# Kernel tuning notes

Measured on AMD Instinct MI355X. Metric: run time of the kernel, lower is better.

The kernel has to match this reference:

```python
import jax, jax.numpy as jnp
import numpy as np

R_SELF = 0.1  # config.r_self from the 'GENERAL' preset


def setup_inputs() -> dict:
    key = jax.random.key(0)
    k1, k2 = jax.random.split(key)
    N, M, D = 16384, 8192, 128
    x = jax.random.uniform(k1, (N, D), dtype=jnp.float32)
    self_samples = jax.random.uniform(k2, (M, D), dtype=jnp.float32)
    return {"x": x, "self_samples": self_samples}


def _cdist(a, b):
    # Euclidean pairwise distances, same math as torch.cdist(p=2).
    a2 = jnp.sum(a * a, axis=1, keepdims=True)          # [N,1]
    b2 = jnp.sum(b * b, axis=1)[None, :]                # [1,M]
    d2 = a2 + b2 - 2.0 * (a @ b.T)                      # [N,M]
    return jnp.sqrt(jnp.maximum(d2, 0.0))


def reference(x, self_samples):
    # get_anomaly_score: min over self set, shifted by r_self, clamped at 0.
    min_dist_to_self = jnp.min(_cdist(x, self_samples), axis=1)  # [N]
    score = jnp.maximum(min_dist_to_self - R_SELF, 0.0)
    return score
```

## Files before the change

kernel.cpp:

```cpp
#include <hip/hip_runtime.h>


using half_t = _Float16;
typedef _Float16 half8 __attribute__((ext_vector_type(8)));
typedef _Float16 half2v __attribute__((ext_vector_type(2)));
typedef float floatx16 __attribute__((ext_vector_type(16)));

#define TILE_ELEMS (128 * 128)

__device__ __forceinline__ void async_load16(const void* g, void* l) {
    __builtin_amdgcn_global_load_lds(
        (const __attribute__((address_space(1))) void*)g,
        (__attribute__((address_space(3))) void*)l, 16, 0, 0);
}

__device__ __forceinline__ void stage_tile(const half_t* __restrict__ Bt,
                                           half_t* __restrict__ dst, int tid) {
    #pragma unroll
    for (int j = 0; j < 4; ++j) {
        int chunk = j * 512 + tid;
        async_load16(Bt + (size_t)chunk * 8, dst + (size_t)chunk * 8);
    }
}

__device__ __forceinline__ half2v h2min(half2v a, half2v b) {
    return __builtin_elementwise_min(a, b);
}

__device__ __forceinline__ half2v pkrtz(float lo, float hi) {
    auto t = __builtin_amdgcn_cvt_pkrtz(lo, hi);
    return __builtin_bit_cast(half2v, t);
}

__global__ __launch_bounds__(256) void prep_kernel(
    const float* __restrict__ x, const float* __restrict__ self,
    half_t* __restrict__ Aws, half_t* __restrict__ Bws,
    float* __restrict__ b2h, float* __restrict__ a2, int Atiles)
{
    __shared__ float part[256];
    int tile = blockIdx.x;
    int tid  = threadIdx.x;
    bool isB = tile >= Atiles;
    int bt   = tile - Atiles;
    const float* src = isB ? (self + (size_t)bt * TILE_ELEMS)
                           : (x    + (size_t)tile * TILE_ELEMS);
    half_t* dst = isB ? (Bws + (size_t)bt * TILE_ELEMS)
                      : (Aws + (size_t)tile * TILE_ELEMS);
    float sgn = isB ? 1.f : -1.f;

    int rowt = tid & 127;
    int k8b  = tid >> 7;
    float ss = 0.f;
    #pragma unroll
    for (int i = 0; i < 8; ++i) {
        int k8 = i * 2 + k8b;
        const float4* p = (const float4*)(src + rowt * 128 + k8 * 8);
        float4 f0 = p[0];
        float4 f1 = p[1];
        half8 h;
        h[0] = (half_t)(sgn * f0.x); h[1] = (half_t)(sgn * f0.y);
        h[2] = (half_t)(sgn * f0.z); h[3] = (half_t)(sgn * f0.w);
        h[4] = (half_t)(sgn * f1.x); h[5] = (half_t)(sgn * f1.y);
        h[6] = (half_t)(sgn * f1.z); h[7] = (half_t)(sgn * f1.w);
        *(half8*)(dst + (size_t)(i * 256 + tid) * 8) = h;
        ss += f0.x*f0.x + f0.y*f0.y + f0.z*f0.z + f0.w*f0.w;
        ss += f1.x*f1.x + f1.y*f1.y + f1.z*f1.z + f1.w*f1.w;
    }
    part[tid] = ss;
    __syncthreads();
    if (tid < 128) {
        float tot = part[tid] + part[tid + 128];
        if (isB) b2h[bt * 128 + tid] = 0.5f * tot;
        else     a2[tile * 128 + tid] = tot;
    }
}

template<int VN>
__device__ __forceinline__ void gemm_iter(
    int t, int iters, int tid, int wc, int ln31, int lh,
    const half_t* __restrict__ Bbase, half_t (*ring)[TILE_ELEMS],
    const float* __restrict__ b2sh,
    const half8 (&areg)[4][8], half2v (&minacc)[4][8])
{
    __builtin_amdgcn_sched_barrier(0);
    if constexpr (VN == 4) asm volatile("s_waitcnt vmcnt(4)" ::: "memory");
    else                   asm volatile("s_waitcnt vmcnt(0)" ::: "memory");
    asm volatile("s_waitcnt lgkmcnt(0)" ::: "memory");
    __builtin_amdgcn_s_barrier();
    __builtin_amdgcn_sched_barrier(0);

    if (t + 2 < iters)
        stage_tile(Bbase + (size_t)(t + 2) * TILE_ELEMS, &ring[(t + 2) % 3][0], tid);

    const half_t* Bs = &ring[t % 3][0];
    float b2v = b2sh[t * 128 + wc * 32 + ln31];

    half8 bf[8];
    #pragma unroll
    for (int ki = 0; ki < 8; ++ki)
        bf[ki] = *(const half8*)(Bs + (size_t)((ki * 2 + lh) * 128 + wc * 32 + ln31) * 8);

    floatx16 c0;
    #pragma unroll
    for (int r = 0; r < 16; ++r) c0[r] = b2v;

    #pragma unroll
    for (int rp = 0; rp < 2; ++rp) {
        floatx16 a0 = __builtin_amdgcn_mfma_f32_32x32x16_f16(areg[rp * 2][0],     bf[0], c0, 0, 0, 0);
        floatx16 a1 = __builtin_amdgcn_mfma_f32_32x32x16_f16(areg[rp * 2 + 1][0], bf[0], c0, 0, 0, 0);
        #pragma unroll
        for (int ki = 1; ki < 8; ++ki) {
            a0 = __builtin_amdgcn_mfma_f32_32x32x16_f16(areg[rp * 2][ki],     bf[ki], a0, 0, 0, 0);
            a1 = __builtin_amdgcn_mfma_f32_32x32x16_f16(areg[rp * 2 + 1][ki], bf[ki], a1, 0, 0, 0);
        }
        #pragma unroll
        for (int i = 0; i < 8; ++i) {
            minacc[rp * 2][i]     = h2min(minacc[rp * 2][i],     pkrtz(a0[2 * i], a0[2 * i + 1]));
            minacc[rp * 2 + 1][i] = h2min(minacc[rp * 2 + 1][i], pkrtz(a1[2 * i], a1[2 * i + 1]));
        }
    }
}

__global__ __launch_bounds__(512, 2) void min_gemm_kernel(
    const half_t* __restrict__ Aws, const half_t* __restrict__ Bws,
    const float* __restrict__ b2h, float* __restrict__ Pmin, int Mslice)
{
    __shared__ half_t ring[3][TILE_ELEMS];
    __shared__ float  b2sh[2048];

    int tid  = threadIdx.x;
    int lane = tid & 63;
    int wid  = tid >> 6;
    int wr   = wid >> 2;
    int wc   = wid & 3;
    int ln31 = lane & 31, lh = lane >> 5;

    const half_t* Atile = Aws + (size_t)(blockIdx.x * 2 + wr) * TILE_ELEMS;
    half8 areg[4][8];
    #pragma unroll
    for (int rt = 0; rt < 4; ++rt)
        #pragma unroll
        for (int ki = 0; ki < 8; ++ki)
            areg[rt][ki] = *(const half8*)(
                Atile + (size_t)((ki * 2 + lh) * 128 + rt * 32 + ln31) * 8);

    int s = blockIdx.y;
    for (int j = tid; j < Mslice; j += 512)
        b2sh[j] = b2h[s * Mslice + j];

    half2v minacc[4][8];
    const half_t HMAX = (half_t)65504.f;
    #pragma unroll
    for (int rt = 0; rt < 4; ++rt)
        #pragma unroll
        for (int i = 0; i < 8; ++i) { minacc[rt][i][0] = HMAX; minacc[rt][i][1] = HMAX; }

    int iters = Mslice >> 7;
    const half_t* Bbase = Bws + (size_t)s * iters * TILE_ELEMS;

    __syncthreads();

    stage_tile(Bbase,              &ring[0][0], tid);
    stage_tile(Bbase + TILE_ELEMS, &ring[1][0], tid);

    for (int t = 0; t < iters - 1; ++t)
        gemm_iter<4>(t, iters, tid, wc, ln31, lh, Bbase, ring, b2sh, areg, minacc);
    gemm_iter<0>(iters - 1, iters, tid, wc, ln31, lh, Bbase, ring, b2sh, areg, minacc);

    #pragma unroll
    for (int rt = 0; rt < 4; ++rt)
        #pragma unroll
        for (int i = 0; i < 8; ++i) {
            int m = __builtin_bit_cast(int, minacc[rt][i]);
            #pragma unroll
            for (int x = 1; x < 32; x <<= 1) {
                int o = __shfl_xor(m, x, 64);
                m = __builtin_bit_cast(int,
                        h2min(__builtin_bit_cast(half2v, m),
                              __builtin_bit_cast(half2v, o)));
            }
            if (ln31 == 0) {
                half2v mv = __builtin_bit_cast(half2v, m);
                int r0 = 2 * i, r1 = 2 * i + 1;
                int rowb = blockIdx.x * 256 + wr * 128 + rt * 32 + 4 * lh;
                int row0 = rowb + (r0 & 3) + 8 * (r0 >> 2);
                int row1 = rowb + (r1 & 3) + 8 * (r1 >> 2);
                Pmin[(size_t)row0 * 16 + s * 4 + wc] = (float)mv[0];
                Pmin[(size_t)row1 * 16 + s * 4 + wc] = (float)mv[1];
            }
        }
}

__global__ __launch_bounds__(256) void final_kernel(
    const float* __restrict__ a2, const float* __restrict__ Pmin,
    float* __restrict__ out)
{
    int row = blockIdx.x * 256 + threadIdx.x;
    const float4* pp = (const float4*)(Pmin + (size_t)row * 16);
    float4 p0 = pp[0];
    float4 p1 = pp[1];
    float4 p2 = pp[2];
    float4 p3 = pp[3];
    float q0 = fminf(fminf(p0.x, p0.y), fminf(p0.z, p0.w));
    float q1 = fminf(fminf(p1.x, p1.y), fminf(p1.z, p1.w));
    float q2 = fminf(fminf(p2.x, p2.y), fminf(p2.z, p2.w));
    float q3 = fminf(fminf(p3.x, p3.y), fminf(p3.z, p3.w));
    float p  = fminf(fminf(q0, q1), fminf(q2, q3));
    float d2 = a2[row] + 2.f * p;
    float d  = sqrtf(fmaxf(d2, 0.f));
    out[row] = fmaxf(d - 0.1f, 0.f);
}

extern "C" void kernel_launch(void* const* d_in, const int* in_sizes, int n_in,
                              void* d_out, int out_size, void* d_ws, size_t ws_size,
                              hipStream_t stream)
{
    const float* x    = (const float*)d_in[0];
    const float* self = (const float*)d_in[1];
    float* out        = (float*)d_out;

    int N = in_sizes[0] / 128;
    int M = in_sizes[1] / 128;
    int Atiles = N / 128;
    int Btiles = M / 128;

    char* w      = (char*)d_ws;
    half_t* Aws  = (half_t*)w;
    half_t* Bws  = Aws + (size_t)N * 128;
    float*  b2h  = (float*)(w + (size_t)(N + M) * 128 * 2);
    float*  Pmin = b2h + M;
    float*  a2   = Pmin + (size_t)N * 16;

    prep_kernel<<<Atiles + Btiles, 256, 0, stream>>>(x, self, Aws, Bws, b2h, a2, Atiles);

    int Mslice = M / 4;
    dim3 grid(N / 256, 4);
    min_gemm_kernel<<<grid, 512, 0, stream>>>(Aws, Bws, b2h, Pmin, Mslice);

    final_kernel<<<N / 256, 256, 0, stream>>>(a2, Pmin, out);
}
```

Before: 103.0 us.

## Double-buffer B fragments in registers, remap block IDs, and raise MFMA priority

```diff
diff --git a/kernel.cpp b/kernel.cpp
--- a/kernel.cpp
+++ b/kernel.cpp
@@ -7,6 +7,7 @@
 typedef float floatx16 __attribute__((ext_vector_type(16)));
 
 #define TILE_ELEMS (128 * 128)
+#define MFMA16 __builtin_amdgcn_mfma_f32_32x32x16_f16
 
 __device__ __forceinline__ void async_load16(const void* g, void* l) {
     __builtin_amdgcn_global_load_lds(
@@ -14,12 +15,12 @@
         (__attribute__((address_space(3))) void*)l, 16, 0, 0);
 }
 
-__device__ __forceinline__ void stage_tile(const half_t* __restrict__ Bt,
-                                           half_t* __restrict__ dst, int tid) {
-    #pragma unroll
-    for (int j = 0; j < 4; ++j) {
-        int chunk = j * 512 + tid;
-        async_load16(Bt + (size_t)chunk * 8, dst + (size_t)chunk * 8);
+__device__ __forceinline__ void stage4(const half_t* __restrict__ Bt,
+                                       half_t* __restrict__ dst, int tid) {
+    #pragma unroll
+    for (int p = 0; p < 4; ++p) {
+        int c = p * 512 + tid;
+        async_load16(Bt + (size_t)c * 8, dst + (size_t)c * 8);
     }
 }
 
@@ -75,50 +76,65 @@
     }
 }
 
-template<int VN>
-__device__ __forceinline__ void gemm_iter(
+__device__ __forceinline__ void body(
     int t, int iters, int tid, int wc, int ln31, int lh,
     const half_t* __restrict__ Bbase, half_t (*ring)[TILE_ELEMS],
     const float* __restrict__ b2sh,
+    half8 (&cur)[8], half8 (&nxt)[8], float& b2v,
     const half8 (&areg)[4][8], half2v (&minacc)[4][8])
 {
-    __builtin_amdgcn_sched_barrier(0);
-    if constexpr (VN == 4) asm volatile("s_waitcnt vmcnt(4)" ::: "memory");
-    else                   asm volatile("s_waitcnt vmcnt(0)" ::: "memory");
+    asm volatile("s_waitcnt vmcnt(0)" ::: "memory");
+    __builtin_amdgcn_sched_barrier(0);
+    __builtin_amdgcn_s_barrier();
+    __builtin_amdgcn_sched_barrier(0);
+
+    if (t + 2 < iters)
+        stage4(Bbase + (size_t)(t + 2) * TILE_ELEMS, &ring[(t + 2) % 3][0], tid);
+
+    float b2vn = b2v;
+    if (t + 1 < iters) {
+        const half_t* Bs = &ring[(t + 1) % 3][0];
+        #pragma unroll
+        for (int ki = 0; ki < 8; ++ki)
+            nxt[ki] = *(const half8*)(Bs + (size_t)((ki * 2 + lh) * 128 + wc * 32 + ln31) * 8);
+        b2vn = b2sh[(t + 1) * 128 + wc * 32 + ln31];
+    }
+
+    const floatx16 ZV = (floatx16)0.0f;
+
+    __builtin_amdgcn_s_setprio(1);
+    floatx16 acc0 = MFMA16(areg[0][0], cur[0], ZV, 0, 0, 0);
+    floatx16 acc1 = MFMA16(areg[1][0], cur[0], ZV, 0, 0, 0);
+    #pragma unroll
+    for (int ki = 1; ki < 8; ++ki) {
+        acc0 = MFMA16(areg[0][ki], cur[ki], acc0, 0, 0, 0);
+        acc1 = MFMA16(areg[1][ki], cur[ki], acc1, 0, 0, 0);
+    }
+    __builtin_amdgcn_s_setprio(0);
+    #pragma unroll
+    for (int i = 0; i < 8; ++i) {
+        minacc[0][i] = h2min(minacc[0][i], pkrtz(acc0[2*i] + b2v, acc0[2*i+1] + b2v));
+        minacc[1][i] = h2min(minacc[1][i], pkrtz(acc1[2*i] + b2v, acc1[2*i+1] + b2v));
+    }
+
+    __builtin_amdgcn_s_setprio(1);
+    floatx16 acc2 = MFMA16(areg[2][0], cur[0], ZV, 0, 0, 0);
+    floatx16 acc3 = MFMA16(areg[3][0], cur[0], ZV, 0, 0, 0);
+    #pragma unroll
+    for (int ki = 1; ki < 8; ++ki) {
+        acc2 = MFMA16(areg[2][ki], cur[ki], acc2, 0, 0, 0);
+        acc3 = MFMA16(areg[3][ki], cur[ki], acc3, 0, 0, 0);
+    }
+    __builtin_amdgcn_s_setprio(0);
+    #pragma unroll
+    for (int i = 0; i < 8; ++i) {
+        minacc[2][i] = h2min(minacc[2][i], pkrtz(acc2[2*i] + b2v, acc2[2*i+1] + b2v));
+        minacc[3][i] = h2min(minacc[3][i], pkrtz(acc3[2*i] + b2v, acc3[2*i+1] + b2v));
+    }
+
     asm volatile("s_waitcnt lgkmcnt(0)" ::: "memory");
-    __builtin_amdgcn_s_barrier();
-    __builtin_amdgcn_sched_barrier(0);
-
-    if (t + 2 < iters)
-        stage_tile(Bbase + (size_t)(t + 2) * TILE_ELEMS, &ring[(t + 2) % 3][0], tid);
-
-    const half_t* Bs = &ring[t % 3][0];
-    float b2v = b2sh[t * 128 + wc * 32 + ln31];
-
-    half8 bf[8];
-    #pragma unroll
-    for (int ki = 0; ki < 8; ++ki)
-        bf[ki] = *(const half8*)(Bs + (size_t)((ki * 2 + lh) * 128 + wc * 32 + ln31) * 8);
-
-    floatx16 c0;
-    #pragma unroll
-    for (int r = 0; r < 16; ++r) c0[r] = b2v;
-
-    #pragma unroll
-    for (int rp = 0; rp < 2; ++rp) {
-        floatx16 a0 = __builtin_amdgcn_mfma_f32_32x32x16_f16(areg[rp * 2][0],     bf[0], c0, 0, 0, 0);
-        floatx16 a1 = __builtin_amdgcn_mfma_f32_32x32x16_f16(areg[rp * 2 + 1][0], bf[0], c0, 0, 0, 0);
-        #pragma unroll
-        for (int ki = 1; ki < 8; ++ki) {
-            a0 = __builtin_amdgcn_mfma_f32_32x32x16_f16(areg[rp * 2][ki],     bf[ki], a0, 0, 0, 0);
-            a1 = __builtin_amdgcn_mfma_f32_32x32x16_f16(areg[rp * 2 + 1][ki], bf[ki], a1, 0, 0, 0);
-        }
-        #pragma unroll
-        for (int i = 0; i < 8; ++i) {
-            minacc[rp * 2][i]     = h2min(minacc[rp * 2][i],     pkrtz(a0[2 * i], a0[2 * i + 1]));
-            minacc[rp * 2 + 1][i] = h2min(minacc[rp * 2 + 1][i], pkrtz(a1[2 * i], a1[2 * i + 1]));
-        }
-    }
+    __builtin_amdgcn_sched_barrier(0);
+    b2v = b2vn;
 }
 
 __global__ __launch_bounds__(512, 2) void min_gemm_kernel(
@@ -135,7 +151,12 @@
     int wc   = wid & 3;
     int ln31 = lane & 31, lh = lane >> 5;
 
-    const half_t* Atile = Aws + (size_t)(blockIdx.x * 2 + wr) * TILE_ELEMS;
+    int id  = blockIdx.x + gridDim.x * blockIdx.y;
+    int swz = (id & 7) * 32 + (id >> 3);
+    int bx  = swz & 63;
+    int s   = swz >> 6;
+
+    const half_t* Atile = Aws + (size_t)(bx * 2 + wr) * TILE_ELEMS;
     half8 areg[4][8];
     #pragma unroll
     for (int rt = 0; rt < 4; ++rt)
@@ -144,8 +165,7 @@
             areg[rt][ki] = *(const half8*)(
                 Atile + (size_t)((ki * 2 + lh) * 128 + rt * 32 + ln31) * 8);
 
-    int s = blockIdx.y;
-    for (int j = tid; j < Mslice; j += 512)
+    for (int j = tid; j < 2048; j += 512)
         b2sh[j] = b2h[s * Mslice + j];
 
     half2v minacc[4][8];
@@ -158,14 +178,24 @@
     int iters = Mslice >> 7;
     const half_t* Bbase = Bws + (size_t)s * iters * TILE_ELEMS;
 
+    stage4(Bbase,              &ring[0][0], tid);
+    stage4(Bbase + TILE_ELEMS, &ring[1][0], tid);
     __syncthreads();
 
-    stage_tile(Bbase,              &ring[0][0], tid);
-    stage_tile(Bbase + TILE_ELEMS, &ring[1][0], tid);
-
-    for (int t = 0; t < iters - 1; ++t)
-        gemm_iter<4>(t, iters, tid, wc, ln31, lh, Bbase, ring, b2sh, areg, minacc);
-    gemm_iter<0>(iters - 1, iters, tid, wc, ln31, lh, Bbase, ring, b2sh, areg, minacc);
+    half8 bfA[8], bfB[8];
+    #pragma unroll
+    for (int ki = 0; ki < 8; ++ki)
+        bfA[ki] = *(const half8*)(&ring[0][0] + (size_t)((ki * 2 + lh) * 128 + wc * 32 + ln31) * 8);
+    float b2v = b2sh[wc * 32 + ln31];
+    asm volatile("s_waitcnt lgkmcnt(0)" ::: "memory");
+    __builtin_amdgcn_sched_barrier(0);
+
+    for (int tt = 0; tt < 8; ++tt) {
+        body(2 * tt,     iters, tid, wc, ln31, lh, Bbase, ring, b2sh,
+             bfA, bfB, b2v, areg, minacc);
+        body(2 * tt + 1, iters, tid, wc, ln31, lh, Bbase, ring, b2sh,
+             bfB, bfA, b2v, areg, minacc);
+    }
 
     #pragma unroll
     for (int rt = 0; rt < 4; ++rt)
@@ -182,7 +212,7 @@
             if (ln31 == 0) {
                 half2v mv = __builtin_bit_cast(half2v, m);
                 int r0 = 2 * i, r1 = 2 * i + 1;
-                int rowb = blockIdx.x * 256 + wr * 128 + rt * 32 + 4 * lh;
+                int rowb = bx * 256 + wr * 128 + rt * 32 + 4 * lh;
                 int row0 = rowb + (r0 & 3) + 8 * (r0 >> 2);
                 int row1 = rowb + (r1 & 3) + 8 * (r1 >> 2);
                 Pmin[(size_t)row0 * 16 + s * 4 + wc] = (float)mv[0];
```

Result: slower. 135.5 us (+31.5%).
